# Kernel tuning notes

Measured on AMD Instinct MI355X. Metric: run time of the kernel, lower is better.

The kernel has to match this reference:

```python
import jax, jax.numpy as jnp
import numpy as np

DIM = 512
NUM_HEADS = 8
HEAD_DIM = DIM // NUM_HEADS
SCALE = HEAD_DIM ** -0.5


def setup_inputs() -> dict:
    key = jax.random.key(0)
    ks = jax.random.split(key, 6)
    B, N, C = 2, 4096, DIM
    s = C ** -0.5  # init scale, torch Linear default-ish
    return {
        "x": jax.random.normal(ks[0], (B, N, C), dtype=jnp.float32),
        "Wq": jax.random.normal(ks[1], (C, C), dtype=jnp.float32) * s,
        "Wk": jax.random.normal(ks[2], (C, C), dtype=jnp.float32) * s,
        "Wv": jax.random.normal(ks[3], (C, C), dtype=jnp.float32) * s,
        "Wo": jax.random.normal(ks[4], (C, C), dtype=jnp.float32) * s,
        "bo": jax.random.normal(ks[5], (C,), dtype=jnp.float32) * s,
    }


def reference(x, Wq, Wk, Wv, Wo, bo):
    B, N, C = x.shape
    H, D = NUM_HEADS, HEAD_DIM
    # torch nn.Linear: y = x @ W.T
    q = (x @ Wq.T).reshape(B, N, H, D).transpose(0, 2, 1, 3)  # [B,H,N,D]
    k = (x @ Wk.T).reshape(B, N, H, D).transpose(0, 2, 1, 3)
    v = (x @ Wv.T).reshape(B, N, H, D).transpose(0, 2, 1, 3)
    attn = jnp.einsum("bhnd,bhmd->bhnm", q, k) * SCALE  # [B,H,N,N]
    attn = jax.nn.softmax(attn, axis=-1)
    out = jnp.einsum("bhnm,bhmd->bhnd", attn, v)
    out = out.transpose(0, 2, 1, 3).reshape(B, N, C)
    return out @ Wo.T + bo
```

## Files before the change

kernel.cpp:

```cpp
#include <hip/hip_runtime.h>
#include <hip/hip_bf16.h>
#include <cstdint>
#include <cstddef>

using bf16 = __bf16;
typedef __attribute__((ext_vector_type(8))) __bf16 bf16x8;
typedef __attribute__((ext_vector_type(4))) float  f32x4;

#define LOG2E 1.4426950408889634f

__device__ inline void gld_lds16(const void* g, void* l) {
  __builtin_amdgcn_global_load_lds(
      (const __attribute__((address_space(1))) void*)g,
      (__attribute__((address_space(3))) void*)l, 16, 0, 0);
}

__global__ __launch_bounds__(256) void k_cvt(const float* __restrict__ s,
                                             bf16* __restrict__ d, int n8) {
  int i = blockIdx.x * 256 + threadIdx.x;
  if (i >= n8) return;
  const float4* p = ((const float4*)s) + (size_t)i * 2;
  float4 a = p[0], b = p[1];
  bf16x8 o;
  o[0] = (bf16)a.x; o[1] = (bf16)a.y; o[2] = (bf16)a.z; o[3] = (bf16)a.w;
  o[4] = (bf16)b.x; o[5] = (bf16)b.y; o[6] = (bf16)b.z; o[7] = (bf16)b.w;
  *(bf16x8*)(d + (size_t)i * 8) = o;
}

__global__ __launch_bounds__(256) void k_cvtw(
    const float* __restrict__ wq, const float* __restrict__ wk,
    const float* __restrict__ wv, const float* __restrict__ wo,
    bf16* __restrict__ wqkv, bf16* __restrict__ wob) {
  int i = blockIdx.x * 256 + threadIdx.x;
  int which = i >> 15, local = i & 32767;
  const float* s = (which == 0) ? wq : (which == 1) ? wk : (which == 2) ? wv : wo;
  bf16* d = (which < 3) ? (wqkv + ((size_t)which << 18)) : wob;
  const float4* p = ((const float4*)s) + (size_t)local * 2;
  float4 a = p[0], b = p[1];
  bf16x8 o;
  o[0] = (bf16)a.x; o[1] = (bf16)a.y; o[2] = (bf16)a.z; o[3] = (bf16)a.w;
  o[4] = (bf16)b.x; o[5] = (bf16)b.y; o[6] = (bf16)b.z; o[7] = (bf16)b.w;
  *(bf16x8*)(d + (size_t)local * 8) = o;
}

__global__ __launch_bounds__(256) void k_gemm(
    const bf16* __restrict__ A, const bf16* __restrict__ B, int mode,
    bf16* __restrict__ Qb, bf16* __restrict__ Kb, bf16* __restrict__ Vtb,
    float* __restrict__ outf, const float* __restrict__ bias) {
  const int K = 512;
  __shared__ alignas(16) bf16 As[128 * 64];
  __shared__ alignas(16) bf16 Bs[128 * 64];
  const int tid = threadIdx.x;
  const int wave = tid >> 6, lane = tid & 63;
  const int l15 = lane & 15, l4 = lane >> 4;
  const int m0 = blockIdx.x * 128, n0 = blockIdx.y * 128;
  const int wr = wave >> 1, wc = wave & 1;
  f32x4 acc[4][4] = {};

  for (int k0 = 0; k0 < K; k0 += 64) {
#pragma unroll
    for (int it = 0; it < 4; ++it) {
      int c = it * 256 + tid;
      int row = c >> 3, kc = c & 7;
      int sb = (kc * 16) ^ ((row & 7) << 4);
      gld_lds16((const char*)A + ((size_t)(m0 + row) * K + k0) * 2 + sb,
                (char*)As + c * 16);
      gld_lds16((const char*)B + ((size_t)(n0 + row) * K + k0) * 2 + sb,
                (char*)Bs + c * 16);
    }
    __syncthreads();
#pragma unroll
    for (int ks = 0; ks < 2; ++ks) {
      bf16x8 af[4], bff[4];
#pragma unroll
      for (int mf = 0; mf < 4; ++mf) {
        int r = wr * 64 + mf * 16 + l15;
        af[mf] = *(const bf16x8*)((const char*)As + r * 128 +
                                  ((ks * 64 + l4 * 16) ^ ((r & 7) << 4)));
      }
#pragma unroll
      for (int nf = 0; nf < 4; ++nf) {
        int r = wc * 64 + nf * 16 + l15;
        bff[nf] = *(const bf16x8*)((const char*)Bs + r * 128 +
                                   ((ks * 64 + l4 * 16) ^ ((r & 7) << 4)));
      }
#pragma unroll
      for (int mf = 0; mf < 4; ++mf)
#pragma unroll
        for (int nf = 0; nf < 4; ++nf)
          acc[mf][nf] = __builtin_amdgcn_mfma_f32_16x16x32_bf16(
              af[mf], bff[nf], acc[mf][nf], 0, 0, 0);
    }
    __syncthreads();
  }

#pragma unroll
  for (int mf = 0; mf < 4; ++mf)
#pragma unroll
    for (int nf = 0; nf < 4; ++nf)
#pragma unroll
      for (int r = 0; r < 4; ++r) {
        int m = m0 + wr * 64 + mf * 16 + l4 * 4 + r;
        int n = n0 + wc * 64 + nf * 16 + l15;
        float v = acc[mf][nf][r];
        if (mode == 1) {
          outf[(size_t)m * 512 + n] = v + bias[n];
        } else {
          int which = n >> 9, o = n & 511, h = o >> 6, d = o & 63;
          int b = m >> 12, nr = m & 4095;
          if (which == 0)
            Qb[((size_t)(b * 8 + h) * 4096 + nr) * 64 + d] = (bf16)(v * 0.125f);
          else if (which == 1)
            Kb[((size_t)(b * 8 + h) * 4096 + nr) * 64 + d] = (bf16)v;
          else
            Vtb[((size_t)((b * 8 + h) * 64 + d)) * 4096 + nr] = (bf16)v;
        }
      }
}

template <int NS>
__global__ __launch_bounds__(256, 4) void k_attn_t(
    const bf16* __restrict__ Q, const bf16* __restrict__ Kg,
    const bf16* __restrict__ Vt, bf16* __restrict__ AO,
    float* __restrict__ pO, float* __restrict__ pD) {
  __shared__ alignas(16) bf16 Ks[64 * 64];
  __shared__ alignas(16) bf16 Vs[64 * 64];
  __shared__ alignas(16) bf16 Ps[4][32 * 64];
  const int tid = threadIdx.x, wave = tid >> 6, lane = tid & 63;
  const int l15 = lane & 15, l4 = lane >> 4;
  const int bh = blockIdx.y, q0 = blockIdx.x * 128;
  const int z = (NS > 1) ? blockIdx.z : 0;
  const int n_lo = z * (4096 / NS);
  const int NT = 4096 / NS / 64;
  const char* Qb = (const char*)(Q + (size_t)bh * 4096 * 64);
  const char* Kb = (const char*)(Kg + (size_t)bh * 4096 * 64);
  const char* Vb = (const char*)(Vt + (size_t)bh * 64 * 4096);

  const int c0 = tid, c1 = 256 + tid;
  const int row0 = c0 >> 3, sb0 = ((c0 & 7) * 16) ^ ((row0 & 7) << 4);
  const int row1 = c1 >> 3, sb1 = ((c1 & 7) * 16) ^ ((row1 & 7) << 4);
  const char* ksrc0 = Kb + (size_t)(n_lo + row0) * 128 + sb0;
  const char* ksrc1 = Kb + (size_t)(n_lo + row1) * 128 + sb1;
  const char* vsrc0 = Vb + (size_t)row0 * 8192 + (size_t)n_lo * 2 + sb0;
  const char* vsrc1 = Vb + (size_t)row1 * 8192 + (size_t)n_lo * 2 + sb1;
  char* kdst0 = (char*)Ks + c0 * 16;
  char* kdst1 = (char*)Ks + c1 * 16;
  char* vdst0 = (char*)Vs + c0 * 16;
  char* vdst1 = (char*)Vs + c1 * 16;

  const char* kf_p[2][4];
#pragma unroll
  for (int cf = 0; cf < 4; ++cf) {
    int kv = cf * 16 + l15;
#pragma unroll
    for (int ds = 0; ds < 2; ++ds)
      kf_p[ds][cf] = (const char*)Ks + kv * 128 +
                     ((ds * 64 + l4 * 16) ^ ((kv & 7) << 4));
  }
  const char* vf_p[4][2];
#pragma unroll
  for (int df = 0; df < 4; ++df) {
    int d = df * 16 + l15;
#pragma unroll
    for (int ks = 0; ks < 2; ++ks)
      vf_p[df][ks] = (const char*)Vs + d * 128 +
                     ((ks * 64 + l4 * 16) ^ ((d & 7) << 4));
  }
  char* pw_p[4][4];
#pragma unroll
  for (int r = 0; r < 4; ++r) {
    int q = l4 * 4 + r;
#pragma unroll
    for (int cf = 0; cf < 4; ++cf)
      pw_p[r][cf] = (char*)Ps[wave] + q * 128 +
                    (((cf * 16 + l15) * 2) ^ ((q & 7) << 4));
  }
  const char* pf_p[2];
#pragma unroll
  for (int ks = 0; ks < 2; ++ks)
    pf_p[ks] = (const char*)Ps[wave] + l15 * 128 +
               ((ks * 64 + l4 * 16) ^ ((l15 & 7) << 4));

  bf16x8 qf[2][2];
#pragma unroll
  for (int mrow = 0; mrow < 2; ++mrow)
#pragma unroll
    for (int ds = 0; ds < 2; ++ds)
      qf[mrow][ds] = *(const bf16x8*)(Qb +
          ((size_t)(q0 + wave * 32 + mrow * 16 + l15) * 64 + ds * 32 + l4 * 8) * 2);

  bf16x8 vone;
#pragma unroll
  for (int j = 0; j < 8; ++j) vone[j] = (bf16)1.0f;

  f32x4 oacc[2][4] = {};
  f32x4 dacc[2] = {};

  for (int t = 0; t < NT; ++t) {
    gld_lds16(ksrc0, kdst0);
    gld_lds16(vsrc0, vdst0);
    gld_lds16(ksrc1, kdst1);
    gld_lds16(vsrc1, vdst1);
    ksrc0 += 8192; ksrc1 += 8192;
    vsrc0 += 128;  vsrc1 += 128;
    __syncthreads();

    f32x4 s[2][4];
#pragma unroll
    for (int cf = 0; cf < 4; ++cf) {
      bf16x8 kf0 = *(const bf16x8*)kf_p[0][cf];
      bf16x8 kf1 = *(const bf16x8*)kf_p[1][cf];
#pragma unroll
      for (int mrow = 0; mrow < 2; ++mrow) {
        f32x4 z2 = {};
        z2 = __builtin_amdgcn_mfma_f32_16x16x32_bf16(qf[mrow][0], kf0, z2, 0, 0, 0);
        z2 = __builtin_amdgcn_mfma_f32_16x16x32_bf16(qf[mrow][1], kf1, z2, 0, 0, 0);
        s[mrow][cf] = z2;
      }
    }

#pragma unroll
    for (int mrow = 0; mrow < 2; ++mrow)
#pragma unroll
      for (int r = 0; r < 4; ++r)
#pragma unroll
        for (int cf = 0; cf < 4; ++cf) {
          float p = __builtin_amdgcn_exp2f(s[mrow][cf][r] * LOG2E);
          *(bf16*)(pw_p[r][cf] + mrow * 2048) = (bf16)p;
        }

    bf16x8 pf[2][2];
#pragma unroll
    for (int mrow = 0; mrow < 2; ++mrow) {
      pf[mrow][0] = *(const bf16x8*)(pf_p[0] + mrow * 2048);
      pf[mrow][1] = *(const bf16x8*)(pf_p[1] + mrow * 2048);
    }

#pragma unroll
    for (int mrow = 0; mrow < 2; ++mrow) {
      dacc[mrow] = __builtin_amdgcn_mfma_f32_16x16x32_bf16(pf[mrow][0], vone,
                                                           dacc[mrow], 0, 0, 0);
      dacc[mrow] = __builtin_amdgcn_mfma_f32_16x16x32_bf16(pf[mrow][1], vone,
                                                           dacc[mrow], 0, 0, 0);
    }

#pragma unroll
    for (int df = 0; df < 4; ++df) {
      bf16x8 vf0 = *(const bf16x8*)vf_p[df][0];
      bf16x8 vf1 = *(const bf16x8*)vf_p[df][1];
#pragma unroll
      for (int mrow = 0; mrow < 2; ++mrow) {
        oacc[mrow][df] = __builtin_amdgcn_mfma_f32_16x16x32_bf16(
            pf[mrow][0], vf0, oacc[mrow][df], 0, 0, 0);
        oacc[mrow][df] = __builtin_amdgcn_mfma_f32_16x16x32_bf16(
            pf[mrow][1], vf1, oacc[mrow][df], 0, 0, 0);
      }
    }
    __syncthreads();
  }

  if (NS > 1) {
    float* po = pO + (((size_t)(z * 16 + bh)) * 4096) * 64;
    float* pd = pD + ((size_t)(z * 16 + bh)) * 4096;
#pragma unroll
    for (int mrow = 0; mrow < 2; ++mrow)
#pragma unroll
      for (int r = 0; r < 4; ++r) {
        int n = q0 + wave * 32 + mrow * 16 + l4 * 4 + r;
#pragma unroll
        for (int df = 0; df < 4; ++df)
          po[(size_t)n * 64 + df * 16 + l15] = oacc[mrow][df][r];
        if (l15 == 0) pd[n] = dacc[mrow][r];
      }
  } else {
    int b = bh >> 3, h = bh & 7;
#pragma unroll
    for (int mrow = 0; mrow < 2; ++mrow)
#pragma unroll
      for (int r = 0; r < 4; ++r) {
        float inv = 1.0f / dacc[mrow][r];
        int n = q0 + wave * 32 + mrow * 16 + l4 * 4 + r;
#pragma unroll
        for (int df = 0; df < 4; ++df) {
          int d = df * 16 + l15;
          AO[((size_t)(b * 4096 + n)) * 512 + h * 64 + d] =
              (bf16)(oacc[mrow][df][r] * inv);
        }
      }
  }
}

template <int NS>
__global__ __launch_bounds__(256) void k_comb(
    const float* __restrict__ pO, const float* __restrict__ pD,
    bf16* __restrict__ AO) {
  const size_t SO = (size_t)16 * 4096 * 64;
  const size_t SD = (size_t)16 * 4096;
  int i = blockIdx.x * 256 + threadIdx.x;
  int g = i >> 3, j = i & 7;
  float den = 0.f;
#pragma unroll
  for (int z = 0; z < NS; ++z) den += pD[g + z * SD];
  float inv = 1.0f / den;
  const float* a = pO + (size_t)g * 64 + j * 8;
  float acc[8] = {};
#pragma unroll
  for (int z = 0; z < NS; ++z)
#pragma unroll
    for (int t = 0; t < 8; ++t) acc[t] += a[z * SO + t];
  bf16x8 o;
#pragma unroll
  for (int t = 0; t < 8; ++t) o[t] = (bf16)(acc[t] * inv);
  int bh = g >> 12, n = g & 4095, b = bh >> 3, h = bh & 7;
  *(bf16x8*)(AO + ((size_t)(b * 4096 + n)) * 512 + h * 64 + j * 8) = o;
}

extern "C" void kernel_launch(void* const* d_in, const int* in_sizes, int n_in,
                              void* d_out, int out_size, void* d_ws,
                              size_t ws_size, hipStream_t stream) {
  const float* x  = (const float*)d_in[0];
  const float* Wq = (const float*)d_in[1];
  const float* Wk = (const float*)d_in[2];
  const float* Wv = (const float*)d_in[3];
  const float* Wo = (const float*)d_in[4];
  const float* bo = (const float*)d_in[5];
  float* out = (float*)d_out;

  char* ws = (char*)d_ws;
  bf16* xb   = (bf16*)(ws);
  bf16* wqkv = (bf16*)(ws + (8u << 20));
  bf16* wob  = (bf16*)(ws + (8u << 20) + 1572864u);
  bf16* Qb   = (bf16*)(ws + (10u << 20));
  bf16* Kb   = (bf16*)(ws + (18u << 20));
  bf16* Vtb  = (bf16*)(ws + (26u << 20));
  bf16* AOb  = (bf16*)(ws + (34u << 20));
  float* pD  = (float*)(ws + (42u << 20));
  float* pO  = (float*)(ws + (43u << 20));

  k_cvt<<<2048, 256, 0, stream>>>(x, xb, 524288);
  k_cvtw<<<512, 256, 0, stream>>>(Wq, Wk, Wv, Wo, wqkv, wob);

  k_gemm<<<dim3(64, 12), 256, 0, stream>>>(xb, wqkv, 0, Qb, Kb, Vtb,
                                           nullptr, nullptr);

  if (ws_size >= ((size_t)108 << 20)) {
    k_attn_t<4><<<dim3(32, 16, 4), 256, 0, stream>>>(Qb, Kb, Vtb, nullptr,
                                                     pO, pD);
    k_comb<4><<<2048, 256, 0, stream>>>(pO, pD, AOb);
  } else if (ws_size >= ((size_t)75 << 20)) {
    k_attn_t<2><<<dim3(32, 16, 2), 256, 0, stream>>>(Qb, Kb, Vtb, nullptr,
                                                     pO, pD);
    k_comb<2><<<2048, 256, 0, stream>>>(pO, pD, AOb);
  } else {
    k_attn_t<1><<<dim3(32, 16), 256, 0, stream>>>(Qb, Kb, Vtb, AOb,
                                                  nullptr, nullptr);
  }

  k_gemm<<<dim3(64, 4), 256, 0, stream>>>(AOb, wob, 1, nullptr, nullptr,
                                          nullptr, out, bo);
}
```

Baseline: 168.0 us.

## Double attention query tile per block and reduce key split to two

Each wave now processes 64 query rows instead of 32, so each block covers 256 queries and reuses each loaded K/V tile across twice as many MFMAs. The key-dimension split drops from four to two, halving partial outputs written and combined. In exchange register use and LDS for P double, occupancy hint falls to 2 blocks per CU, and the grid shrinks to 512 blocks, reducing latency hiding.

```diff
diff --git a/kernel.cpp b/kernel.cpp
--- a/kernel.cpp
+++ b/kernel.cpp
@@ -119,16 +119,16 @@
 }
 
 template <int NS>
-__global__ __launch_bounds__(256, 4) void k_attn_t(
+__global__ __launch_bounds__(256, 2) void k_attn_t(
     const bf16* __restrict__ Q, const bf16* __restrict__ Kg,
     const bf16* __restrict__ Vt, bf16* __restrict__ AO,
     float* __restrict__ pO, float* __restrict__ pD) {
   __shared__ alignas(16) bf16 Ks[64 * 64];
   __shared__ alignas(16) bf16 Vs[64 * 64];
-  __shared__ alignas(16) bf16 Ps[4][32 * 64];
+  __shared__ alignas(16) bf16 Ps[4][64 * 64];
   const int tid = threadIdx.x, wave = tid >> 6, lane = tid & 63;
   const int l15 = lane & 15, l4 = lane >> 4;
-  const int bh = blockIdx.y, q0 = blockIdx.x * 128;
+  const int bh = blockIdx.y, q0 = blockIdx.x * 256;
   const int z = (NS > 1) ? blockIdx.z : 0;
   const int n_lo = z * (4096 / NS);
   const int NT = 4096 / NS / 64;
@@ -181,20 +181,20 @@
     pf_p[ks] = (const char*)Ps[wave] + l15 * 128 +
                ((ks * 64 + l4 * 16) ^ ((l15 & 7) << 4));
 
-  bf16x8 qf[2][2];
-#pragma unroll
-  for (int mrow = 0; mrow < 2; ++mrow)
+  bf16x8 qf[4][2];
+#pragma unroll
+  for (int mr = 0; mr < 4; ++mr)
 #pragma unroll
     for (int ds = 0; ds < 2; ++ds)
-      qf[mrow][ds] = *(const bf16x8*)(Qb +
-          ((size_t)(q0 + wave * 32 + mrow * 16 + l15) * 64 + ds * 32 + l4 * 8) * 2);
+      qf[mr][ds] = *(const bf16x8*)(Qb +
+          ((size_t)(q0 + wave * 64 + mr * 16 + l15) * 64 + ds * 32 + l4 * 8) * 2);
 
   bf16x8 vone;
 #pragma unroll
   for (int j = 0; j < 8; ++j) vone[j] = (bf16)1.0f;
 
-  f32x4 oacc[2][4] = {};
-  f32x4 dacc[2] = {};
+  f32x4 oacc[4][4] = {};
+  f32x4 dacc[4] = {};
 
   for (int t = 0; t < NT; ++t) {
     gld_lds16(ksrc0, kdst0);
@@ -205,43 +205,43 @@
     vsrc0 += 128;  vsrc1 += 128;
     __syncthreads();
 
-    f32x4 s[2][4];
+    f32x4 s[4][4];
 #pragma unroll
     for (int cf = 0; cf < 4; ++cf) {
       bf16x8 kf0 = *(const bf16x8*)kf_p[0][cf];
       bf16x8 kf1 = *(const bf16x8*)kf_p[1][cf];
 #pragma unroll
-      for (int mrow = 0; mrow < 2; ++mrow) {
+      for (int mr = 0; mr < 4; ++mr) {
         f32x4 z2 = {};
-        z2 = __builtin_amdgcn_mfma_f32_16x16x32_bf16(qf[mrow][0], kf0, z2, 0, 0, 0);
-        z2 = __builtin_amdgcn_mfma_f32_16x16x32_bf16(qf[mrow][1], kf1, z2, 0, 0, 0);
-        s[mrow][cf] = z2;
-      }
-    }
-
-#pragma unroll
-    for (int mrow = 0; mrow < 2; ++mrow)
+        z2 = __builtin_amdgcn_mfma_f32_16x16x32_bf16(qf[mr][0], kf0, z2, 0, 0, 0);
+        z2 = __builtin_amdgcn_mfma_f32_16x16x32_bf16(qf[mr][1], kf1, z2, 0, 0, 0);
+        s[mr][cf] = z2;
+      }
+    }
+
+#pragma unroll
+    for (int mr = 0; mr < 4; ++mr)
 #pragma unroll
       for (int r = 0; r < 4; ++r)
 #pragma unroll
         for (int cf = 0; cf < 4; ++cf) {
-          float p = __builtin_amdgcn_exp2f(s[mrow][cf][r] * LOG2E);
-          *(bf16*)(pw_p[r][cf] + mrow * 2048) = (bf16)p;
+          float p = __builtin_amdgcn_exp2f(s[mr][cf][r] * LOG2E);
+          *(bf16*)(pw_p[r][cf] + mr * 2048) = (bf16)p;
         }
 
-    bf16x8 pf[2][2];
-#pragma unroll
-    for (int mrow = 0; mrow < 2; ++mrow) {
-      pf[mrow][0] = *(const bf16x8*)(pf_p[0] + mrow * 2048);
-      pf[mrow][1] = *(const bf16x8*)(pf_p[1] + mrow * 2048);
-    }
-
-#pragma unroll
-    for (int mrow = 0; mrow < 2; ++mrow) {
-      dacc[mrow] = __builtin_amdgcn_mfma_f32_16x16x32_bf16(pf[mrow][0], vone,
-                                                           dacc[mrow], 0, 0, 0);
-      dacc[mrow] = __builtin_amdgcn_mfma_f32_16x16x32_bf16(pf[mrow][1], vone,
-                                                           dacc[mrow], 0, 0, 0);
+    bf16x8 pf[4][2];
+#pragma unroll
+    for (int mr = 0; mr < 4; ++mr) {
+      pf[mr][0] = *(const bf16x8*)(pf_p[0] + mr * 2048);
+      pf[mr][1] = *(const bf16x8*)(pf_p[1] + mr * 2048);
+    }
+
+#pragma unroll
+    for (int mr = 0; mr < 4; ++mr) {
+      dacc[mr] = __builtin_amdgcn_mfma_f32_16x16x32_bf16(pf[mr][0], vone,
+                                                         dacc[mr], 0, 0, 0);
+      dacc[mr] = __builtin_amdgcn_mfma_f32_16x16x32_bf16(pf[mr][1], vone,
+                                                         dacc[mr], 0, 0, 0);
     }
 
 #pragma unroll
@@ -249,11 +249,11 @@
       bf16x8 vf0 = *(const bf16x8*)vf_p[df][0];
       bf16x8 vf1 = *(const bf16x8*)vf_p[df][1];
 #pragma unroll
-      for (int mrow = 0; mrow < 2; ++mrow) {
-        oacc[mrow][df] = __builtin_amdgcn_mfma_f32_16x16x32_bf16(
-            pf[mrow][0], vf0, oacc[mrow][df], 0, 0, 0);
-        oacc[mrow][df] = __builtin_amdgcn_mfma_f32_16x16x32_bf16(
-            pf[mrow][1], vf1, oacc[mrow][df], 0, 0, 0);
+      for (int mr = 0; mr < 4; ++mr) {
+        oacc[mr][df] = __builtin_amdgcn_mfma_f32_16x16x32_bf16(
+            pf[mr][0], vf0, oacc[mr][df], 0, 0, 0);
+        oacc[mr][df] = __builtin_amdgcn_mfma_f32_16x16x32_bf16(
+            pf[mr][1], vf1, oacc[mr][df], 0, 0, 0);
       }
     }
     __syncthreads();
@@ -263,28 +263,28 @@
     float* po = pO + (((size_t)(z * 16 + bh)) * 4096) * 64;
     float* pd = pD + ((size_t)(z * 16 + bh)) * 4096;
 #pragma unroll
-    for (int mrow = 0; mrow < 2; ++mrow)
+    for (int mr = 0; mr < 4; ++mr)
 #pragma unroll
       for (int r = 0; r < 4; ++r) {
-        int n = q0 + wave * 32 + mrow * 16 + l4 * 4 + r;
+        int n = q0 + wave * 64 + mr * 16 + l4 * 4 + r;
 #pragma unroll
         for (int df = 0; df < 4; ++df)
-          po[(size_t)n * 64 + df * 16 + l15] = oacc[mrow][df][r];
-        if (l15 == 0) pd[n] = dacc[mrow][r];
+          po[(size_t)n * 64 + df * 16 + l15] = oacc[mr][df][r];
+        if (l15 == 0) pd[n] = dacc[mr][r];
       }
   } else {
     int b = bh >> 3, h = bh & 7;
 #pragma unroll
-    for (int mrow = 0; mrow < 2; ++mrow)
+    for (int mr = 0; mr < 4; ++mr)
 #pragma unroll
       for (int r = 0; r < 4; ++r) {
-        float inv = 1.0f / dacc[mrow][r];
-        int n = q0 + wave * 32 + mrow * 16 + l4 * 4 + r;
+        float inv = 1.0f / dacc[mr][r];
+        int n = q0 + wave * 64 + mr * 16 + l4 * 4 + r;
 #pragma unroll
         for (int df = 0; df < 4; ++df) {
           int d = df * 16 + l15;
           AO[((size_t)(b * 4096 + n)) * 512 + h * 64 + d] =
-              (bf16)(oacc[mrow][df][r] * inv);
+              (bf16)(oacc[mr][df][r] * inv);
         }
       }
   }
@@ -343,16 +343,12 @@
   k_gemm<<<dim3(64, 12), 256, 0, stream>>>(xb, wqkv, 0, Qb, Kb, Vtb,
                                            nullptr, nullptr);
 
-  if (ws_size >= ((size_t)108 << 20)) {
-    k_attn_t<4><<<dim3(32, 16, 4), 256, 0, stream>>>(Qb, Kb, Vtb, nullptr,
-                                                     pO, pD);
-    k_comb<4><<<2048, 256, 0, stream>>>(pO, pD, AOb);
-  } else if (ws_size >= ((size_t)75 << 20)) {
-    k_attn_t<2><<<dim3(32, 16, 2), 256, 0, stream>>>(Qb, Kb, Vtb, nullptr,
+  if (ws_size >= ((size_t)75 << 20)) {
+    k_attn_t<2><<<dim3(16, 16, 2), 256, 0, stream>>>(Qb, Kb, Vtb, nullptr,
                                                      pO, pD);
     k_comb<2><<<2048, 256, 0, stream>>>(pO, pD, AOb);
   } else {
-    k_attn_t<1><<<dim3(32, 16), 256, 0, stream>>>(Qb, Kb, Vtb, AOb,
+    k_attn_t<1><<<dim3(16, 16), 256, 0, stream>>>(Qb, Kb, Vtb, AOb,
                                                   nullptr, nullptr);
   }
 
```

Measured after the change: 171.6 us. 1.02x slower.
